# Kernel tuning notes

Measured on AMD Instinct MI355X. Metric: run time of the kernel, lower is better.

The kernel has to match this reference:

```python
import jax, jax.numpy as jnp
import numpy as np

IN_OCT = 512
OUT_OCT = 512
BATCH = 512


def setup_inputs() -> dict:
    key = jax.random.key(0)
    kx, kw = jax.random.split(key)
    x = jax.random.normal(kx, (BATCH, IN_OCT * 8), dtype=jnp.float32)
    weight = jax.random.normal(kw, (OUT_OCT, IN_OCT, 8, 8), dtype=jnp.float32)
    bias = jnp.zeros((OUT_OCT, 8), dtype=jnp.float32)
    return {"x": x, "weight": weight, "bias": bias}


def reference(x, weight, bias):
    # x: [B, in_oct*8]; weight: [out_oct, in_oct, 8, 8]; bias: [out_oct, 8]
    B = x.shape[0]
    out_oct, in_oct = weight.shape[0], weight.shape[1]
    xo = x.reshape(B, in_oct, 8)
    # octonion_mul(x[:, j], weight[i, j]) applies the per-pair 8x8 octonion
    # left-multiplication matrix; summed over j it is one bilinear contraction.
    y = jnp.einsum("bjp,ijpk->bik", xo, weight) + bias[None, :, :]
    return y.reshape(B, out_oct * 8)
```

## Files before the change

### kernel.cpp

```cpp
#include <hip/hip_runtime.h>
#include <stdint.h>


#define M_DIM 512
#define N_DIM 4096
#define K_DIM 4096
#define KSPLIT 4
#define NIT ((K_DIM / KSPLIT) / 32)
#define PART_ELEMS (M_DIM * N_DIM)

typedef __bf16 bf16x8 __attribute__((ext_vector_type(8)));
typedef float f32x4 __attribute__((ext_vector_type(4)));

__device__ inline unsigned short f2bf(float f) {
  union { float f; unsigned int u; } v;
  v.f = f;
  unsigned int u = v.u;
  unsigned int r = (u + 0x7fffu + ((u >> 16) & 1u)) >> 16;
  return (unsigned short)r;
}

__global__ __launch_bounds__(256) void prep_kernel(
    const float* __restrict__ x, const float* __restrict__ w,
    const float* __restrict__ bias, unsigned short* __restrict__ abf,
    unsigned short* __restrict__ bt, float* __restrict__ out) {
  const int bid = blockIdx.x;
  const int t = threadIdx.x;
  if (bid < 4096) {
    __shared__ __align__(16) unsigned short lT[8][512];
    const int i = bid >> 3;
    const int jg = bid & 7;
    const float4* src =
        (const float4*)(w + (size_t)i * 32768 + jg * 4096 + t * 16);
    float4 v0 = src[0], v1 = src[1], v2 = src[2], v3 = src[3];
    const int jp = (t >> 2) * 8 + (t & 3) * 2;
    const float* lo = (const float*)&v0;
    const float* hi = (const float*)&v2;
#pragma unroll
    for (int k = 0; k < 4; ++k) {
      unsigned int pk =
          (unsigned int)f2bf(lo[k]) | ((unsigned int)f2bf(hi[k]) << 16);
      *(unsigned int*)&lT[k][jp] = pk;
    }
    lo = (const float*)&v1;
    hi = (const float*)&v3;
#pragma unroll
    for (int k = 0; k < 4; ++k) {
      unsigned int pk =
          (unsigned int)f2bf(lo[k]) | ((unsigned int)f2bf(hi[k]) << 16);
      *(unsigned int*)&lT[k + 4][jp] = pk;
    }
    __syncthreads();
    const int r = t >> 5, c = t & 31;
    const uint4* s = (const uint4*)&lT[r][c * 16];
    uint4* d = (uint4*)(bt + (size_t)(i * 8 + r) * K_DIM + jg * 512 + c * 16);
    d[0] = s[0];
    d[1] = s[1];
  } else if (bid < 5120) {
    int g = (bid - 4096) * 256 + t;
    const float4* xi = (const float4*)x;
    float4 a = xi[g * 2];
    float4 b = xi[g * 2 + 1];
    __attribute__((aligned(16))) unsigned short o[8] = {
        f2bf(a.x), f2bf(a.y), f2bf(a.z), f2bf(a.w),
        f2bf(b.x), f2bf(b.y), f2bf(b.z), f2bf(b.w)};
    *(uint4*)(abf + (size_t)g * 8) = *(const uint4*)o;
  } else {
    int g = (bid - 5120) * 256 + t;
    int el = g * 4;
    int col = el & (N_DIM - 1);
    *(float4*)(out + el) = *(const float4*)(bias + col);
  }
}

__device__ inline void gld16(const void* g, void* l) {
  __builtin_amdgcn_global_load_lds(
      (const __attribute__((address_space(1))) unsigned int*)g,
      (__attribute__((address_space(3))) unsigned int*)l, 16, 0, 0);
}

__global__ __launch_bounds__(512, 4) void gemm_kernel(
    const unsigned short* __restrict__ A, const unsigned short* __restrict__ Bt,
    float* __restrict__ out, float* __restrict__ part, int use_atomic) {
  __shared__ __align__(16) char lds[2][16 * 1024];
  const int t = threadIdx.x;
  const int n0 = blockIdx.x * 128;
  const int m0 = blockIdx.y * 128;
  const int z = blockIdx.z;
  const int kc0 = z * (K_DIM / KSPLIT);
  const int w = t >> 6;
  const int lane = t & 63;
  const int wr = w >> 2;
  const int wc = w & 3;
  const int lrow = lane & 15;
  const int kb = lane >> 4;

  f32x4 acc[4][2] = {};

  const size_t aOff = (size_t)(m0 + (t >> 2)) * K_DIM + kc0 + (t & 3) * 8;
  const size_t bOff = (size_t)(n0 + (t >> 2)) * K_DIM + kc0 + (t & 3) * 8;

  auto issue = [&](int it) {
    char* buf = lds[it & 1];
    gld16(A + aOff + it * 32, buf + t * 16);
    gld16(Bt + bOff + it * 32, buf + 8192 + t * 16);
  };

  issue(0);
  for (int it = 0; it < NIT; ++it) {
    __syncthreads();
    if (it + 1 < NIT) issue(it + 1);
    const unsigned short* cA = (const unsigned short*)lds[it & 1];
    const unsigned short* cB = cA + 4096;

    bf16x8 af[4], bfr[2];
#pragma unroll
    for (int mt = 0; mt < 4; ++mt)
      af[mt] = *(const bf16x8*)(cA + (wr * 64 + mt * 16 + lrow) * 32 + kb * 8);
#pragma unroll
    for (int nt = 0; nt < 2; ++nt)
      bfr[nt] = *(const bf16x8*)(cB + (wc * 32 + nt * 16 + lrow) * 32 + kb * 8);
#pragma unroll
    for (int mt = 0; mt < 4; ++mt)
#pragma unroll
      for (int nt = 0; nt < 2; ++nt)
        acc[mt][nt] = __builtin_amdgcn_mfma_f32_16x16x32_bf16(
            af[mt], bfr[nt], acc[mt][nt], 0, 0, 0);
  }

#pragma unroll
  for (int mt = 0; mt < 4; ++mt) {
    const int gmb = m0 + wr * 64 + mt * 16 + kb * 4;
#pragma unroll
    for (int nt = 0; nt < 2; ++nt) {
      const int gn = n0 + wc * 32 + nt * 16 + lrow;
      if (use_atomic) {
#pragma unroll
        for (int r = 0; r < 4; ++r)
          atomicAdd(out + (size_t)(gmb + r) * N_DIM + gn, acc[mt][nt][r]);
      } else {
        float* p = part + (size_t)z * PART_ELEMS;
#pragma unroll
        for (int r = 0; r < 4; ++r)
          p[(size_t)(gmb + r) * N_DIM + gn] = acc[mt][nt][r];
      }
    }
  }
}

__global__ __launch_bounds__(256) void reduce_kernel(
    const float* __restrict__ part, const float* __restrict__ bias,
    float* __restrict__ out) {
  const int g = blockIdx.x * 256 + threadIdx.x;
  const float4* p = (const float4*)part;
  const float4* b4 = (const float4*)bias;
  const int Q = PART_ELEMS / 4;
  float4 s0 = p[g];
  float4 s1 = p[g + Q];
  float4 s2 = p[g + 2 * Q];
  float4 s3 = p[g + 3 * Q];
  float4 bb = b4[g & (N_DIM / 4 - 1)];
  float4 r;
  r.x = s0.x + s1.x + s2.x + s3.x + bb.x;
  r.y = s0.y + s1.y + s2.y + s3.y + bb.y;
  r.z = s0.z + s1.z + s2.z + s3.z + bb.z;
  r.w = s0.w + s1.w + s2.w + s3.w + bb.w;
  ((float4*)out)[g] = r;
}

extern "C" void kernel_launch(void* const* d_in, const int* in_sizes, int n_in,
                              void* d_out, int out_size, void* d_ws,
                              size_t ws_size, hipStream_t stream) {
  const float* x = (const float*)d_in[0];
  const float* w = (const float*)d_in[1];
  const float* bias = (const float*)d_in[2];
  float* out = (float*)d_out;

  unsigned short* abf = (unsigned short*)d_ws;
  unsigned short* bt = abf + (size_t)M_DIM * K_DIM;
  float* part = (float*)((char*)d_ws + 36u * 1024 * 1024);

  const bool have_ws = ws_size >= 68ull * 1024 * 1024;
  const int use_atomic = have_ws ? 0 : 1;

  prep_kernel<<<use_atomic ? 7168 : 5120, 256, 0, stream>>>(x, w, bias, abf,
                                                            bt, out);

  dim3 grid(N_DIM / 128, M_DIM / 128, KSPLIT);
  gemm_kernel<<<grid, 512, 0, stream>>>(abf, bt, out, part, use_atomic);

  if (!use_atomic)
    reduce_kernel<<<PART_ELEMS / 4 / 256, 256, 0, stream>>>(part, bias, out);
}
```

Measured before the change: 139.0 us.

## Fuse split-K reduction into GEMM via per-tile arrival counter

Removes the separate reduce kernel. Each GEMM block writes its split-K partial, fences, and increments a per-output-tile atomic counter. The last arriving block sums the four partials plus bias for its 128x128 tile. Counters are zeroed in the prep kernel. This saves a kernel launch and lets the reduction overlap with other GEMM blocks, at the cost of extra fences, an atomic per block, and a tail of serial reduction work on the last blocks.

```diff
diff --git a/kernel.cpp b/kernel.cpp
--- a/kernel.cpp
+++ b/kernel.cpp
@@ -8,6 +8,7 @@
 #define KSPLIT 4
 #define NIT ((K_DIM / KSPLIT) / 32)
 #define PART_ELEMS (M_DIM * N_DIM)
+#define N_TILES ((N_DIM / 128) * (M_DIM / 128))
 
 typedef __bf16 bf16x8 __attribute__((ext_vector_type(8)));
 typedef float f32x4 __attribute__((ext_vector_type(4)));
@@ -23,7 +24,8 @@
 __global__ __launch_bounds__(256) void prep_kernel(
     const float* __restrict__ x, const float* __restrict__ w,
     const float* __restrict__ bias, unsigned short* __restrict__ abf,
-    unsigned short* __restrict__ bt, float* __restrict__ out) {
+    unsigned short* __restrict__ bt, float* __restrict__ out,
+    int* __restrict__ cnt) {
   const int bid = blockIdx.x;
   const int t = threadIdx.x;
   if (bid < 4096) {
@@ -57,6 +59,7 @@
     d[0] = s[0];
     d[1] = s[1];
   } else if (bid < 5120) {
+    if (bid == 4096 && t < N_TILES) cnt[t] = 0;
     int g = (bid - 4096) * 256 + t;
     const float4* xi = (const float4*)x;
     float4 a = xi[g * 2];
@@ -81,7 +84,8 @@
 
 __global__ __launch_bounds__(512, 4) void gemm_kernel(
     const unsigned short* __restrict__ A, const unsigned short* __restrict__ Bt,
-    float* __restrict__ out, float* __restrict__ part, int use_atomic) {
+    const float* __restrict__ bias, float* __restrict__ out,
+    float* __restrict__ part, int* __restrict__ cnt, int use_atomic) {
   __shared__ __align__(16) char lds[2][16 * 1024];
   const int t = threadIdx.x;
   const int n0 = blockIdx.x * 128;
@@ -128,44 +132,69 @@
             af[mt], bfr[nt], acc[mt][nt], 0, 0, 0);
   }
 
+  if (use_atomic) {
+#pragma unroll
+    for (int mt = 0; mt < 4; ++mt) {
+      const int gmb = m0 + wr * 64 + mt * 16 + kb * 4;
+#pragma unroll
+      for (int nt = 0; nt < 2; ++nt) {
+        const int gn = n0 + wc * 32 + nt * 16 + lrow;
+#pragma unroll
+        for (int r = 0; r < 4; ++r)
+          atomicAdd(out + (size_t)(gmb + r) * N_DIM + gn, acc[mt][nt][r]);
+      }
+    }
+    return;
+  }
+
+  float* p = part + (size_t)z * PART_ELEMS;
 #pragma unroll
   for (int mt = 0; mt < 4; ++mt) {
     const int gmb = m0 + wr * 64 + mt * 16 + kb * 4;
 #pragma unroll
     for (int nt = 0; nt < 2; ++nt) {
       const int gn = n0 + wc * 32 + nt * 16 + lrow;
-      if (use_atomic) {
-#pragma unroll
-        for (int r = 0; r < 4; ++r)
-          atomicAdd(out + (size_t)(gmb + r) * N_DIM + gn, acc[mt][nt][r]);
-      } else {
-        float* p = part + (size_t)z * PART_ELEMS;
-#pragma unroll
-        for (int r = 0; r < 4; ++r)
-          p[(size_t)(gmb + r) * N_DIM + gn] = acc[mt][nt][r];
-      }
-    }
-  }
-}
-
-__global__ __launch_bounds__(256) void reduce_kernel(
-    const float* __restrict__ part, const float* __restrict__ bias,
-    float* __restrict__ out) {
-  const int g = blockIdx.x * 256 + threadIdx.x;
-  const float4* p = (const float4*)part;
+#pragma unroll
+      for (int r = 0; r < 4; ++r)
+        p[(size_t)(gmb + r) * N_DIM + gn] = acc[mt][nt][r];
+    }
+  }
+  __threadfence();
+
+  __shared__ int lastFlag;
+  if (t == 0) {
+    const int tile = blockIdx.y * (N_DIM / 128) + blockIdx.x;
+    int old = __hip_atomic_fetch_add(&cnt[tile], 1, __ATOMIC_ACQ_REL,
+                                     __HIP_MEMORY_SCOPE_AGENT);
+    lastFlag = (old == KSPLIT - 1);
+  }
+  __syncthreads();
+  if (!lastFlag) return;
+  __threadfence();
+
+  const float4* pp = (const float4*)part;
   const float4* b4 = (const float4*)bias;
-  const int Q = PART_ELEMS / 4;
-  float4 s0 = p[g];
-  float4 s1 = p[g + Q];
-  float4 s2 = p[g + 2 * Q];
-  float4 s3 = p[g + 3 * Q];
-  float4 bb = b4[g & (N_DIM / 4 - 1)];
-  float4 r;
-  r.x = s0.x + s1.x + s2.x + s3.x + bb.x;
-  r.y = s0.y + s1.y + s2.y + s3.y + bb.y;
-  r.z = s0.z + s1.z + s2.z + s3.z + bb.z;
-  r.w = s0.w + s1.w + s2.w + s3.w + bb.w;
-  ((float4*)out)[g] = r;
+  float4* o4 = (float4*)out;
+  const int NQ = N_DIM / 4;
+  const int PQ = PART_ELEMS / 4;
+#pragma unroll
+  for (int i = 0; i < 8; ++i) {
+    const int fl = i * 512 + t;
+    const int row = fl >> 5;
+    const int col = fl & 31;
+    const size_t base = (size_t)(m0 + row) * NQ + (n0 >> 2) + col;
+    float4 s0 = pp[base];
+    float4 s1 = pp[base + PQ];
+    float4 s2 = pp[base + 2 * PQ];
+    float4 s3 = pp[base + 3 * PQ];
+    float4 bb = b4[(n0 >> 2) + col];
+    float4 r;
+    r.x = s0.x + s1.x + s2.x + s3.x + bb.x;
+    r.y = s0.y + s1.y + s2.y + s3.y + bb.y;
+    r.z = s0.z + s1.z + s2.z + s3.z + bb.z;
+    r.w = s0.w + s1.w + s2.w + s3.w + bb.w;
+    o4[base] = r;
+  }
 }
 
 extern "C" void kernel_launch(void* const* d_in, const int* in_sizes, int n_in,
@@ -179,16 +208,15 @@
   unsigned short* abf = (unsigned short*)d_ws;
   unsigned short* bt = abf + (size_t)M_DIM * K_DIM;
   float* part = (float*)((char*)d_ws + 36u * 1024 * 1024);
-
-  const bool have_ws = ws_size >= 68ull * 1024 * 1024;
+  int* cnt = (int*)((char*)d_ws + 68u * 1024 * 1024);
+
+  const bool have_ws = ws_size >= 69ull * 1024 * 1024;
   const int use_atomic = have_ws ? 0 : 1;
 
   prep_kernel<<<use_atomic ? 7168 : 5120, 256, 0, stream>>>(x, w, bias, abf,
-                                                            bt, out);
+                                                            bt, out, cnt);
 
   dim3 grid(N_DIM / 128, M_DIM / 128, KSPLIT);
-  gemm_kernel<<<grid, 512, 0, stream>>>(abf, bt, out, part, use_atomic);
-
-  if (!use_atomic)
-    reduce_kernel<<<PART_ELEMS / 4 / 256, 256, 0, stream>>>(part, bias, out);
-}
+  gemm_kernel<<<grid, 512, 0, stream>>>(abf, bt, bias, out, part, cnt,
+                                        use_atomic);
+}
```

Result: slower. 309.5 us (+122.7%).
